# Optimization experiments

Measured on AMD Instinct MI355X. Metric: run time of the kernel, lower is better.

Reference implementation:

```python
import jax, jax.numpy as jnp
import numpy as np


def _rope_tables(seq_len, d_k, dtype):
    # Faithful to SimpleRotary intent: only d_k//4 frequencies exist; the
    # remaining d_k//4 of the half-width table is identity (cos=1, sin=0),
    # i.e. zero angular frequency (modded-nanogpt style partial rotary).
    half = d_k // 2
    quarter = d_k // 4
    freqs = (1.0 / 10000.0) ** np.linspace(0.0, 1.0, quarter, dtype=np.float32)
    ang = np.concatenate([freqs, np.zeros(half - quarter, dtype=np.float32)])
    theta = np.arange(seq_len, dtype=np.float32)[:, None] * ang[None, :]  # [S, d_k//2]
    return jnp.asarray(np.cos(theta), dtype), jnp.asarray(np.sin(theta), dtype)


def _apply_rope(x, cos, sin):
    # x: [B, H, S, d_k]; cos/sin: [S, d_k//2]
    x1, x2 = jnp.split(x, 2, axis=-1)
    c = cos[None, None]  # [1,1,S,d_k//2]
    s = sin[None, None]
    return jnp.concatenate([x1 * c - x2 * s, x1 * s + x2 * c], axis=-1)


def setup_inputs() -> dict:
    key = jax.random.key(0)
    k1, k2, k3 = jax.random.split(key, 3)
    B, S, D = 2, 2048, 1024
    x = jax.random.normal(k1, (B, S, D), dtype=jnp.float32)
    Wqkv = jax.random.normal(k2, (3 * D, D), dtype=jnp.float32) * 0.02
    Wo = jax.random.normal(k3, (D, D), dtype=jnp.float32) * 0.02
    return {"x": x, "Wqkv": Wqkv, "Wo": Wo, "n_heads": 16}


def reference(x, Wqkv, Wo, n_heads):
    B, S, D = x.shape
    d_k = D // n_heads
    qkv = jnp.einsum('bsd,ed->bse', x, Wqkv)  # [B,S,3D]
    qkv = qkv.reshape(B, S, 3, n_heads, d_k).transpose(2, 0, 3, 1, 4)  # [3,B,H,S,d_k]
    q, k, v = qkv[0], qkv[1], qkv[2]
    cos, sin = _rope_tables(S, d_k, x.dtype)
    q = _apply_rope(q, cos, sin)
    k = _apply_rope(k, cos, sin)
    scale = 1.0 / float(np.sqrt(d_k))
    scores = jnp.einsum('bhqd,bhkd->bhqk', q, k) * scale  # [B,H,S,S]
    causal = jnp.tril(jnp.ones((S, S), dtype=bool))
    scores = jnp.where(causal[None, None], scores, jnp.finfo(scores.dtype).min)
    probs = jax.nn.softmax(scores, axis=-1)
    out = jnp.einsum('bhqk,bhkd->bhqd', probs, v)  # [B,H,S,d_k]
    out = out.transpose(0, 2, 1, 3).reshape(B, S, D)
    return jnp.einsum('bsd,ed->bse', out, Wo)
```

## Files before the change

kernel.cpp:

```cpp
#include <hip/hip_runtime.h>
#include <hip/hip_bf16.h>


typedef __bf16 bf16x8 __attribute__((ext_vector_type(8)));
typedef float f32x4 __attribute__((ext_vector_type(4)));

#define LOG2E 1.4426950408889634f

__device__ __forceinline__ ushort f2bf(float f) {
  __hip_bfloat16 h = __float2bfloat16(f);
  return __builtin_bit_cast(ushort, h);
}

__device__ __forceinline__ uint pack2(float a, float b) {
  return (uint)f2bf(a) | ((uint)f2bf(b) << 16);
}

__device__ __forceinline__ uint pack2t(float a, float b) {
  return __builtin_amdgcn_perm(__builtin_bit_cast(uint, b),
                               __builtin_bit_cast(uint, a), 0x07060302u);
}

__device__ __forceinline__ float fexp2(float x) {
#if __has_builtin(__builtin_amdgcn_exp2f)
  return __builtin_amdgcn_exp2f(x);
#else
  float r;
  asm volatile("v_exp_f32 %0, %1\n\ts_nop 0" : "=v"(r) : "v"(x));
  return r;
#endif
}

#define CBAR() __asm__ __volatile__("" ::: "memory")

__device__ __forceinline__ void gl2lds16(const ushort* g, ushort* l) {
  __builtin_amdgcn_global_load_lds(
      (const __attribute__((address_space(1))) void*)g,
      (__attribute__((address_space(3))) void*)l, 16, 0, 0);
}

__global__ __launch_bounds__(256) void conv_bf16(const float* __restrict__ src,
                                                 ushort* __restrict__ dst,
                                                 int n8) {
  int i = blockIdx.x * 256 + threadIdx.x;
  if (i >= n8) return;
  const float4* s = (const float4*)src + (long)i * 2;
  float4 a = s[0], b = s[1];
  uint4 pk = {pack2(a.x, a.y), pack2(a.z, a.w), pack2(b.x, b.y), pack2(b.z, b.w)};
  ((uint4*)dst)[i] = pk;
}

__global__ __launch_bounds__(256) void gemm_bt(
    const ushort* __restrict__ A, const ushort* __restrict__ B, int nbn,
    ushort* __restrict__ qb, ushort* __restrict__ kb, ushort* __restrict__ vb,
    float* __restrict__ Cout, int epi) {
  __shared__ __align__(16) ushort SMEM[17408];
  ushort* As = SMEM;
  ushort* Bs = SMEM + 8192;
  const int tid = threadIdx.x;
  const int w = tid >> 6, lane = tid & 63, quad = lane >> 4, lc = lane & 15;
  const int bid = blockIdx.x;
  const int bm = bid / nbn, bn = bid % nbn;
  const int wm = (w & 1) * 64, wn = (w >> 1) * 64;

  f32x4 acc[4][4] = {};

  const ushort* Ag = A + (long)bm * 131072;
  const ushort* Bg = B + (long)bn * 131072;

  for (int k0 = 0; k0 < 1024; k0 += 64) {
    __syncthreads();
    for (int i = 0; i < 4; ++i) {
      int u = i * 256 + tid;
      int row = u >> 3, ch = u & 7;
      gl2lds16(Ag + row * 1024 + k0 + ch * 8, &As[(i * 256 + w * 64) * 8]);
      gl2lds16(Bg + row * 1024 + k0 + ch * 8, &Bs[(i * 256 + w * 64) * 8]);
    }
    __builtin_amdgcn_s_waitcnt(0);
    __syncthreads();
    for (int kc = 0; kc < 2; ++kc) {
      bf16x8 af[4], bfr[4];
      for (int t = 0; t < 4; ++t)
        af[t] = *(const bf16x8*)&As[(wm + t * 16 + lc) * 64 + kc * 32 + quad * 8];
      for (int t = 0; t < 4; ++t)
        bfr[t] = *(const bf16x8*)&Bs[(wn + t * 16 + lc) * 64 + kc * 32 + quad * 8];
      for (int rt = 0; rt < 4; ++rt)
        for (int ct = 0; ct < 4; ++ct)
          acc[rt][ct] = __builtin_amdgcn_mfma_f32_16x16x32_bf16(
              af[rt], bfr[ct], acc[rt][ct], 0, 0, 0);
    }
  }

  if (epi == 0) {
    const int e0 = bn * 128;
    const int g = e0 >> 10;
    const int h0 = (e0 & 1023) >> 6;
    ushort* Ct = SMEM;
    __syncthreads();

    if (g == 2) {
      for (int rt = 0; rt < 4; ++rt)
        for (int ct = 0; ct < 4; ++ct) {
          int col = wn + ct * 16 + lc;
          int r0 = wm + rt * 16 + quad * 4;
          uint2 pk = {pack2(acc[rt][ct][0], acc[rt][ct][1]),
                      pack2(acc[rt][ct][2], acc[rt][ct][3])};
          *(uint2*)&Ct[col * 136 + r0] = pk;
        }
    } else {
      const float qs = (g == 0) ? 0.125f * LOG2E : 1.0f;
      const float ang = powf(1e-4f, (float)lc * (1.0f / 15.0f));
      for (int rt = 0; rt < 4; ++rt)
        for (int r = 0; r < 4; ++r) {
          int row = wm + rt * 16 + quad * 4 + r;
          int srow = (bm * 128 + row) & 2047;
          float theta = (float)srow * ang;
          float sn, c;
          sincosf(theta, &sn, &c);
          float x1 = acc[rt][0][r], x2 = acc[rt][2][r];
          acc[rt][0][r] = x1 * c - x2 * sn;
          acc[rt][2][r] = x1 * sn + x2 * c;
          for (int ct = 0; ct < 4; ++ct)
            Ct[row * 136 + wn + ct * 16 + lc] = f2bf(acc[rt][ct][r] * qs);
        }
    }
    __syncthreads();

    if (g == 0) {
      for (int i = 0; i < 8; ++i) {
        int u = i * 256 + tid;
        int row = u >> 4, c8 = u & 15;
        int m = bm * 128 + row;
        int srow = m & 2047, b = m >> 11;
        uint4 vv = *(const uint4*)&Ct[row * 136 + c8 * 8];
        *(uint4*)&qb[(((long)(b * 16 + h0 + (c8 >> 3))) * 2048 + srow) * 64 +
                     (c8 & 7) * 8] = vv;
      }
    } else if (g == 1) {
      for (int i = 0; i < 8; ++i) {
        int u = i * 256 + tid;
        int head = u >> 10, off = u & 1023;
        int jrel = off >> 9, kc = (off >> 8) & 1, t = (off >> 6) & 3;
        int quadK = (off >> 4) & 3, lcA = off & 15;
        int srl = jrel * 64 + t * 16 + lcA;
        uint4 vv = *(const uint4*)&Ct[srl * 136 + head * 64 + kc * 32 + quadK * 8];
        int m = bm * 128 + srl;
        int srow = m & 2047, b = m >> 11;
        int bh = b * 16 + h0 + head;
        int chunk = (srow >> 6) * 8 + kc * 4 + t;
        *(uint4*)&kb[(long)bh * 131072 + chunk * 512 + (quadK * 16 + lcA) * 8] = vv;
      }
    } else {
      for (int i = 0; i < 8; ++i) {
        int u = i * 256 + tid;
        int head = u >> 10, off = u & 1023;
        int jrel = off >> 9, kcV = (off >> 8) & 1, mt = (off >> 6) & 3;
        int quadV = (off >> 4) & 3, lcA = off & 15;
        int srl = jrel * 64 + kcV * 32 + quadV * 8;
        int d = mt * 16 + lcA;
        uint4 vv = *(const uint4*)&Ct[(head * 64 + d) * 136 + srl];
        int m = bm * 128 + srl;
        int srow = m & 2047, b = m >> 11;
        int bh = b * 16 + h0 + head;
        int chunk = (srow >> 6) * 8 + kcV * 4 + mt;
        *(uint4*)&vb[(long)bh * 131072 + chunk * 512 + (quadV * 16 + lcA) * 8] = vv;
      }
    }
  } else {
    const int row0 = bm * 128 + wm;
    for (int rt = 0; rt < 4; ++rt)
      for (int r = 0; r < 4; ++r) {
        int m = row0 + rt * 16 + quad * 4 + r;
        float* drow = Cout + (long)m * 1024 + bn * 128 + wn;
        for (int ct = 0; ct < 4; ++ct)
          drow[ct * 16 + lc] = acc[rt][ct][r];
      }
  }
}

__global__ __launch_bounds__(64) void attn_kernel(
    const ushort* __restrict__ qb, const ushort* __restrict__ kb,
    const ushort* __restrict__ vt, ushort* __restrict__ out) {
  __shared__ __align__(16) ushort Psw2[2][32 * 64];
  const int lane = threadIdx.x;
  const int quad = lane >> 4, lc = lane & 15, l7 = lc & 7;
  const int bid = blockIdx.x;
  const int s = 63 - (bid >> 5);
  const int bh = bid & 31;
  const int bidx = bh >> 4, h = bh & 15;
  const int qtbase = s * 32;

  bf16x8 qf[2][2];
  for (int kc = 0; kc < 2; ++kc)
    for (int q2 = 0; q2 < 2; ++q2)
      qf[kc][q2] = *(const bf16x8*)&qb[((long)bh * 2048 + qtbase + q2 * 16 + lc) * 64 +
                                       kc * 32 + quad * 8];

  f32x4 oacc[4][2] = {};
  float l_lane[2] = {0.0f, 0.0f};

  const ushort* K = kb + (long)bh * 131072;
  const ushort* Vt = vt + (long)bh * 131072;
  const int jmax = s >> 1;
  const int rowoff = (s & 1) * 32;
  const int lane8 = lane * 8;

#define LOADTILE(KF, VF, JT)                                                   \
  {                                                                            \
    const ushort* Kp_ = K + (JT) * 4096 + lane8;                               \
    const ushort* Vp_ = Vt + (JT) * 4096 + lane8;                              \
    for (int kc = 0; kc < 2; ++kc)                                             \
      for (int t = 0; t < 4; ++t) {                                            \
        KF[kc][t] = *(const bf16x8*)&Kp_[(kc * 4 + t) * 512];                  \
        VF[kc][t] = *(const bf16x8*)&Vp_[(kc * 4 + t) * 512];                  \
      }                                                                        \
  }

#define COMPUTE(KF, VF, J, PAR)                                                \
  {                                                                            \
    f32x4 sacc[4][2] = {};                                                     \
    for (int kc = 0; kc < 2; ++kc)                                             \
      for (int kt = 0; kt < 4; ++kt)                                           \
        for (int q2 = 0; q2 < 2; ++q2)                                         \
          sacc[kt][q2] = __builtin_amdgcn_mfma_f32_16x16x32_bf16(              \
              KF[kc][kt], qf[kc][q2], sacc[kt][q2], 0, 0, 0);                  \
    if ((J) == jmax) {                                \
      for (int kt = 0; kt < 4; ++kt)                                           \
        for (int q2 = 0; q2 < 2; ++q2) {                                       \
          int rowrel = rowoff + q2 * 16 + lc;                                  \
          for (int r = 0; r < 4; ++r)                                          \
            if (kt * 16 + quad * 4 + r > rowrel) sacc[kt][q2][r] = -1.0e30f;   \
        }                                                                      \
    }                                                                          \
    ushort* Psw = Psw2[PAR];                                                   \
    for (int q2 = 0; q2 < 2; ++q2) {                                           \
      float p[4][4];                                                           \
      float rs = 0.0f;                                                         \
      for (int kt = 0; kt < 4; ++kt)                                           \
        for (int r = 0; r < 4; ++r) {                                          \
          p[kt][r] = fexp2(sacc[kt][q2][r]);                                   \
          rs += p[kt][r];                                                      \
        }                                                                      \
      l_lane[q2] += rs;                                                        \
      for (int kt = 0; kt < 4; ++kt) {                                         \
        uint2 pk = {pack2t(p[kt][0], p[kt][1]), pack2t(p[kt][2], p[kt][3])};   \
        *(uint2*)&Psw[(q2 * 16 + lc) * 64 +                                    \
                      (((kt * 2 + (quad >> 1)) ^ l7) << 3) +                   \
                      ((quad & 1) << 2)] = pk;                                 \
      }                                                                        \
    }                                                                          \
    CBAR();       \
    for (int kc = 0; kc < 2; ++kc) {                                           \
      bf16x8 pf[2];                                                            \
      for (int q2 = 0; q2 < 2; ++q2)                                           \
        pf[q2] = *(const bf16x8*)&Psw[(q2 * 16 + lc) * 64 +                    \
                                      (((kc * 4 + quad) ^ l7) << 3)];          \
      for (int mt = 0; mt < 4; ++mt)                                           \
        for (int q2 = 0; q2 < 2; ++q2)                                         \
          oacc[mt][q2] = __builtin_amdgcn_mfma_f32_16x16x32_bf16(              \
              VF[kc][mt], pf[q2], oacc[mt][q2], 0, 0, 0);                      \
    }                                                                          \
  }

  bf16x8 kA[2][4], vA[2][4], kB[2][4], vB[2][4];
  LOADTILE(kA, vA, 0);
  int j = 0;
  while (true) {
    int jn = (j < jmax) ? j + 1 : j;
    LOADTILE(kB, vB, jn);
    COMPUTE(kA, vA, j, 0);
    if (j >= jmax) break;
    ++j;
    int jn2 = (j < jmax) ? j + 1 : j;
    LOADTILE(kA, vA, jn2);
    COMPUTE(kB, vB, j, 1);
    if (j >= jmax) break;
    ++j;
  }
#undef LOADTILE
#undef COMPUTE

  float l_[2];
  for (int q2 = 0; q2 < 2; ++q2) {
    float rs = l_lane[q2];
    rs += __shfl_xor(rs, 16, 64);
    rs += __shfl_xor(rs, 32, 64);
    l_[q2] = rs;
  }
  ushort* Psw = Psw2[0];
  CBAR();
  for (int q2 = 0; q2 < 2; ++q2) {
    float linv = 1.0f / l_[q2];
    for (int mt = 0; mt < 4; ++mt) {
      uint2 pk = {pack2(oacc[mt][q2][0] * linv, oacc[mt][q2][1] * linv),
                  pack2(oacc[mt][q2][2] * linv, oacc[mt][q2][3] * linv)};
      *(uint2*)&Psw[(q2 * 16 + lc) * 64 + (((mt * 2 + (quad >> 1)) ^ l7) << 3) +
                    ((quad & 1) << 2)] = pk;
    }
  }
  CBAR();
  {
    int r2 = lane >> 1;
    long mrow = (long)bidx * 2048 + qtbase + r2;
    for (int c = 0; c < 4; ++c) {
      int c8 = (lane & 1) * 4 + c;
      uint4 vv = *(const uint4*)&Psw[r2 * 64 + ((c8 ^ (r2 & 7)) << 3)];
      *(uint4*)&out[mrow * 1024 + h * 64 + c8 * 8] = vv;
    }
  }
}

extern "C" void kernel_launch(void* const* d_in, const int* in_sizes, int n_in,
                              void* d_out, int out_size, void* d_ws, size_t ws_size,
                              hipStream_t stream) {
  const float* x = nullptr;
  const float* Wqkv = nullptr;
  const float* Wo = nullptr;
  for (int i = 0; i < n_in; ++i) {
    if (in_sizes[i] == 4194304) x = (const float*)d_in[i];
    else if (in_sizes[i] == 3145728) Wqkv = (const float*)d_in[i];
    else if (in_sizes[i] == 1048576) Wo = (const float*)d_in[i];
  }
  float* out = (float*)d_out;

  ushort* qbuf = (ushort*)d_ws;
  ushort* kbuf = qbuf + 4194304;
  ushort* vbuf = kbuf + 4194304;
  ushort* scr4 = vbuf + 4194304;
  ushort* wqkvh = scr4;
  ushort* ao   = scr4;
  ushort* woh  = qbuf;
  ushort* xh   = (ushort*)d_out;

  conv_bf16<<<2048, 256, 0, stream>>>(x, xh, 524288);
  conv_bf16<<<1536, 256, 0, stream>>>(Wqkv, wqkvh, 393216);
  gemm_bt<<<768, 256, 0, stream>>>(xh, wqkvh, 24, qbuf, kbuf, vbuf, nullptr, 0);
  attn_kernel<<<2048, 64, 0, stream>>>(qbuf, kbuf, vbuf, ao);
  conv_bf16<<<512, 256, 0, stream>>>(Wo, woh, 131072);
  gemm_bt<<<256, 256, 0, stream>>>(ao, woh, 8, nullptr, nullptr, nullptr, out, 1);
}
```

Baseline: 196.6 us.

## Pre-swizzle GEMM operands into MFMA fragment layout and load directly to registers

The bf16 conversion kernels now write x, Wqkv and Wo in a 16-row by 32-column MFMA fragment-tiled layout, and the x and Wqkv conversions are merged into one launch. Both GEMMs then load fragments straight from global memory into registers with double buffering, dropping the LDS staging and its barriers. The output projection gets its own 64-thread, 64x64-tile kernel that stages results in LDS for coalesced float4 stores. Attention writes its output in the same fragment layout and raises wave priority around its MFMA blocks. The risks are losing LDS-based reuse across waves, which raises global and L2 traffic, and lower occupancy in the small-workgroup projection GEMM.

```diff
diff --git a/kernel.cpp b/kernel.cpp
--- a/kernel.cpp
+++ b/kernel.cpp
@@ -33,30 +33,42 @@
 
 #define CBAR() __asm__ __volatile__("" ::: "memory")
 
-__device__ __forceinline__ void gl2lds16(const ushort* g, ushort* l) {
-  __builtin_amdgcn_global_load_lds(
-      (const __attribute__((address_space(1))) void*)g,
-      (__attribute__((address_space(3))) void*)l, 16, 0, 0);
-}
-
-__global__ __launch_bounds__(256) void conv_bf16(const float* __restrict__ src,
+__device__ __forceinline__ void conv_frag_one(const float* __restrict__ src,
+                                              ushort* __restrict__ dst, int i) {
+  int row = i >> 7, cc = i & 127;
+  int r16 = row >> 4, rr = row & 15;
+  int k32 = cc >> 2, quad = cc & 3;
+  const float4* s = (const float4*)src + (long)i * 2;
+  float4 a = s[0], b = s[1];
+  uint4 pk = {pack2(a.x, a.y), pack2(a.z, a.w), pack2(b.x, b.y), pack2(b.z, b.w)};
+  *(uint4*)&dst[((long)r16 * 32 + k32) * 512 + (quad * 16 + rr) * 8] = pk;
+}
+
+__global__ __launch_bounds__(256) void conv_frag(const float* __restrict__ src,
                                                  ushort* __restrict__ dst,
                                                  int n8) {
   int i = blockIdx.x * 256 + threadIdx.x;
   if (i >= n8) return;
-  const float4* s = (const float4*)src + (long)i * 2;
-  float4 a = s[0], b = s[1];
-  uint4 pk = {pack2(a.x, a.y), pack2(a.z, a.w), pack2(b.x, b.y), pack2(b.z, b.w)};
-  ((uint4*)dst)[i] = pk;
+  conv_frag_one(src, dst, i);
+}
+
+__global__ __launch_bounds__(256) void conv_frag2(
+    const float* __restrict__ s0, ushort* __restrict__ d0, int n0,
+    const float* __restrict__ s1, ushort* __restrict__ d1, int n1) {
+  int i = blockIdx.x * 256 + threadIdx.x;
+  if (i < n0) {
+    conv_frag_one(s0, d0, i);
+  } else {
+    i -= n0;
+    if (i >= n1) return;
+    conv_frag_one(s1, d1, i);
+  }
 }
 
 __global__ __launch_bounds__(256) void gemm_bt(
     const ushort* __restrict__ A, const ushort* __restrict__ B, int nbn,
-    ushort* __restrict__ qb, ushort* __restrict__ kb, ushort* __restrict__ vb,
-    float* __restrict__ Cout, int epi) {
+    ushort* __restrict__ qb, ushort* __restrict__ kb, ushort* __restrict__ vb) {
   __shared__ __align__(16) ushort SMEM[17408];
-  ushort* As = SMEM;
-  ushort* Bs = SMEM + 8192;
   const int tid = threadIdx.x;
   const int w = tid >> 6, lane = tid & 63, quad = lane >> 4, lc = lane & 15;
   const int bid = blockIdx.x;
@@ -65,33 +77,35 @@
 
   f32x4 acc[4][4] = {};
 
-  const ushort* Ag = A + (long)bm * 131072;
-  const ushort* Bg = B + (long)bn * 131072;
-
-  for (int k0 = 0; k0 < 1024; k0 += 64) {
-    __syncthreads();
-    for (int i = 0; i < 4; ++i) {
-      int u = i * 256 + tid;
-      int row = u >> 3, ch = u & 7;
-      gl2lds16(Ag + row * 1024 + k0 + ch * 8, &As[(i * 256 + w * 64) * 8]);
-      gl2lds16(Bg + row * 1024 + k0 + ch * 8, &Bs[(i * 256 + w * 64) * 8]);
-    }
-    __builtin_amdgcn_s_waitcnt(0);
-    __syncthreads();
-    for (int kc = 0; kc < 2; ++kc) {
-      bf16x8 af[4], bfr[4];
-      for (int t = 0; t < 4; ++t)
-        af[t] = *(const bf16x8*)&As[(wm + t * 16 + lc) * 64 + kc * 32 + quad * 8];
-      for (int t = 0; t < 4; ++t)
-        bfr[t] = *(const bf16x8*)&Bs[(wn + t * 16 + lc) * 64 + kc * 32 + quad * 8];
-      for (int rt = 0; rt < 4; ++rt)
-        for (int ct = 0; ct < 4; ++ct)
-          acc[rt][ct] = __builtin_amdgcn_mfma_f32_16x16x32_bf16(
-              af[rt], bfr[ct], acc[rt][ct], 0, 0, 0);
-    }
-  }
-
-  if (epi == 0) {
+  const ushort* Ap = A + (long)(bm * 8 + (w & 1) * 4) * 16384 + lane * 8;
+  const ushort* Bp = B + (long)(bn * 8 + (w >> 1) * 4) * 16384 + lane * 8;
+
+#define GLD(AF, BF, K32)                                                       \
+  {                                                                            \
+    for (int t = 0; t < 4; ++t)                                                \
+      AF[t] = *(const bf16x8*)&Ap[(long)t * 16384 + (K32) * 512];              \
+    for (int t = 0; t < 4; ++t)                                                \
+      BF[t] = *(const bf16x8*)&Bp[(long)t * 16384 + (K32) * 512];              \
+  }
+#define MM(AF, BF)                                                             \
+  for (int rt = 0; rt < 4; ++rt)                                               \
+    for (int ct = 0; ct < 4; ++ct)                                             \
+      acc[rt][ct] = __builtin_amdgcn_mfma_f32_16x16x32_bf16(                   \
+          AF[rt], BF[ct], acc[rt][ct], 0, 0, 0);
+
+  bf16x8 a0[4], b0[4], a1[4], b1[4];
+  GLD(a0, b0, 0);
+  for (int k = 0; k < 32; k += 2) {
+    GLD(a1, b1, k + 1);
+    MM(a0, b0);
+    int kn = (k + 2 < 32) ? k + 2 : 31;
+    GLD(a0, b0, kn);
+    MM(a1, b1);
+  }
+#undef GLD
+#undef MM
+
+  {
     const int e0 = bn * 128;
     const int g = e0 >> 10;
     const int h0 = (e0 & 1023) >> 6;
@@ -166,15 +180,56 @@
         *(uint4*)&vb[(long)bh * 131072 + chunk * 512 + (quadV * 16 + lcA) * 8] = vv;
       }
     }
-  } else {
-    const int row0 = bm * 128 + wm;
-    for (int rt = 0; rt < 4; ++rt)
-      for (int r = 0; r < 4; ++r) {
-        int m = row0 + rt * 16 + quad * 4 + r;
-        float* drow = Cout + (long)m * 1024 + bn * 128 + wn;
-        for (int ct = 0; ct < 4; ++ct)
-          drow[ct * 16 + lc] = acc[rt][ct][r];
-      }
+  }
+}
+
+__global__ __launch_bounds__(64) void gemm_proj(
+    const ushort* __restrict__ A, const ushort* __restrict__ B,
+    float* __restrict__ Cout) {
+  __shared__ __align__(16) float T[64 * 68];
+  const int lane = threadIdx.x, quad = lane >> 4, lc = lane & 15;
+  const int bid = blockIdx.x;
+  const int bm = bid >> 4, bn = bid & 15;
+
+  f32x4 acc[4][4] = {};
+
+  const ushort* Ap = A + (long)(bm * 4) * 16384 + lane * 8;
+  const ushort* Bp = B + (long)(bn * 4) * 16384 + lane * 8;
+
+#define GLD(AF, BF, K32)                                                       \
+  {                                                                            \
+    for (int t = 0; t < 4; ++t)                                                \
+      AF[t] = *(const bf16x8*)&Ap[(long)t * 16384 + (K32) * 512];              \
+    for (int t = 0; t < 4; ++t)                                                \
+      BF[t] = *(const bf16x8*)&Bp[(long)t * 16384 + (K32) * 512];              \
+  }
+#define MM(AF, BF)                                                             \
+  for (int rt = 0; rt < 4; ++rt)                                               \
+    for (int ct = 0; ct < 4; ++ct)                                             \
+      acc[rt][ct] = __builtin_amdgcn_mfma_f32_16x16x32_bf16(                   \
+          AF[rt], BF[ct], acc[rt][ct], 0, 0, 0);
+
+  bf16x8 a0[4], b0[4], a1[4], b1[4];
+  GLD(a0, b0, 0);
+  for (int k = 0; k < 32; k += 2) {
+    GLD(a1, b1, k + 1);
+    MM(a0, b0);
+    int kn = (k + 2 < 32) ? k + 2 : 31;
+    GLD(a0, b0, kn);
+    MM(a1, b1);
+  }
+#undef GLD
+#undef MM
+
+  for (int rt = 0; rt < 4; ++rt)
+    for (int ct = 0; ct < 4; ++ct)
+      for (int r = 0; r < 4; ++r)
+        T[(rt * 16 + quad * 4 + r) * 68 + ct * 16 + lc] = acc[rt][ct][r];
+  CBAR();
+  for (int p = 0; p < 16; ++p) {
+    int row = p * 4 + quad;
+    float4 v = *(const float4*)&T[row * 68 + lc * 4];
+    *(float4*)&Cout[(long)(bm * 64 + row) * 1024 + bn * 64 + lc * 4] = v;
   }
 }
 
@@ -219,11 +274,13 @@
 #define COMPUTE(KF, VF, J, PAR)                                                \
   {                                                                            \
     f32x4 sacc[4][2] = {};                                                     \
+    __builtin_amdgcn_s_setprio(1);                                             \
     for (int kc = 0; kc < 2; ++kc)                                             \
       for (int kt = 0; kt < 4; ++kt)                                           \
         for (int q2 = 0; q2 < 2; ++q2)                                         \
           sacc[kt][q2] = __builtin_amdgcn_mfma_f32_16x16x32_bf16(              \
               KF[kc][kt], qf[kc][q2], sacc[kt][q2], 0, 0, 0);                  \
+    __builtin_amdgcn_s_setprio(0);                                             \
     if ((J) == jmax) {                                \
       for (int kt = 0; kt < 4; ++kt)                                           \
         for (int q2 = 0; q2 < 2; ++q2) {                                       \
@@ -250,6 +307,7 @@
       }                                                                        \
     }                                                                          \
     CBAR();       \
+    __builtin_amdgcn_s_setprio(1);                                             \
     for (int kc = 0; kc < 2; ++kc) {                                           \
       bf16x8 pf[2];                                                            \
       for (int q2 = 0; q2 < 2; ++q2)                                           \
@@ -260,6 +318,7 @@
           oacc[mt][q2] = __builtin_amdgcn_mfma_f32_16x16x32_bf16(              \
               VF[kc][mt], pf[q2], oacc[mt][q2], 0, 0, 0);                      \
     }                                                                          \
+    __builtin_amdgcn_s_setprio(0);                                             \
   }
 
   bf16x8 kA[2][4], vA[2][4], kB[2][4], vB[2][4];
@@ -301,11 +360,13 @@
   CBAR();
   {
     int r2 = lane >> 1;
-    long mrow = (long)bidx * 2048 + qtbase + r2;
+    long m = (long)bidx * 2048 + qtbase + r2;
+    int m4 = (int)(m >> 4), rr = (int)(m & 15);
     for (int c = 0; c < 4; ++c) {
       int c8 = (lane & 1) * 4 + c;
       uint4 vv = *(const uint4*)&Psw[r2 * 64 + ((c8 ^ (r2 & 7)) << 3)];
-      *(uint4*)&out[mrow * 1024 + h * 64 + c8 * 8] = vv;
+      *(uint4*)&out[((long)m4 * 32 + h * 2 + (c8 >> 2)) * 512 +
+                    ((c8 & 3) * 16 + rr) * 8] = vv;
     }
   }
 }
@@ -332,10 +393,9 @@
   ushort* woh  = qbuf;
   ushort* xh   = (ushort*)d_out;
 
-  conv_bf16<<<2048, 256, 0, stream>>>(x, xh, 524288);
-  conv_bf16<<<1536, 256, 0, stream>>>(Wqkv, wqkvh, 393216);
-  gemm_bt<<<768, 256, 0, stream>>>(xh, wqkvh, 24, qbuf, kbuf, vbuf, nullptr, 0);
+  conv_frag2<<<3584, 256, 0, stream>>>(x, xh, 524288, Wqkv, wqkvh, 393216);
+  gemm_bt<<<768, 256, 0, stream>>>(xh, wqkvh, 24, qbuf, kbuf, vbuf);
   attn_kernel<<<2048, 64, 0, stream>>>(qbuf, kbuf, vbuf, ao);
-  conv_bf16<<<512, 256, 0, stream>>>(Wo, woh, 131072);
-  gemm_bt<<<256, 256, 0, stream>>>(ao, woh, 8, nullptr, nullptr, nullptr, out, 1);
-}
+  conv_frag<<<512, 256, 0, stream>>>(Wo, woh, 131072);
+  gemm_proj<<<1024, 64, 0, stream>>>(ao, woh, out);
+}
```

Measured after the change: 196.1 us. Within noise of the previous version (-0.2%).
